# Kernel optimization log

Hardware: AMD Instinct MI355X
Metric: run time of the kernel (lower is better)

## Reference

```python
import jax, jax.numpy as jnp
import numpy as np

B, S, D, K, T = 8, 1024, 128, 16, 8  # batch, seq_len, dim, stack_size, recursion depth
N = B * S                            # per-token stack memory batch
RESIDUAL = 0.1                       # cfg.RESIDUAL_WEIGHT
EPS = 1e-6                           # cfg.EPSILON
SCALE = D ** -0.5


def _clinear(zr, zi, Wr, Wi):
    # (zr + i*zi) @ (Wr + i*Wi); W stored [in, out] (torch Linear weight transposed)
    return zr @ Wr - zi @ Wi, zi @ Wr + zr @ Wi


def _cattn(zr, zi, p):
    # ComplexAttention: complex q/k/v, softmax over concat([real, imag]) scores
    Wqr, Wqi, Wkr, Wki, Wvr, Wvi = p
    qr, qi = _clinear(zr, zi, Wqr, Wqi)
    kr, ki = _clinear(zr, zi, Wkr, Wki)
    vr, vi = _clinear(zr, zi, Wvr, Wvi)
    qf = jnp.concatenate([qr, qi], -1)
    kf = jnp.concatenate([kr, ki], -1)
    a = jax.nn.softmax(jnp.einsum('...id,...jd->...ij', qf, kf) * SCALE, -1)
    return jnp.einsum('...ij,...jd->...id', a, vr), jnp.einsum('...ij,...jd->...id', a, vi)


def setup_inputs() -> dict:
    key = jax.random.key(0)
    ks = jax.random.split(key, 18)
    mk = lambda k: jax.random.normal(k, (D, D), jnp.float32) * (D ** -0.5)
    inp = {
        'x_real': jax.random.normal(ks[0], (B, S, D), jnp.float32),
        'x_imag': jax.random.normal(ks[1], (B, S, D), jnp.float32),
        # sequence ComplexAttention weights
        'Wq_r': mk(ks[2]), 'Wq_i': mk(ks[3]),
        'Wk_r': mk(ks[4]), 'Wk_i': mk(ks[5]),
        'Wv_r': mk(ks[6]), 'Wv_i': mk(ks[7]),
        # stack-memory ComplexAttention weights
        'Mq_r': mk(ks[8]), 'Mq_i': mk(ks[9]),
        'Mk_r': mk(ks[10]), 'Mk_i': mk(ks[11]),
        'Mv_r': mk(ks[12]), 'Mv_i': mk(ks[13]),
        # ctrl projection (push/pop/stay logits) and output modulus projection
        'Wc': jax.random.normal(ks[14], (2 * D, 3), jnp.float32) * 0.05,
        'bc': jnp.zeros((3,), jnp.float32),
        'Wo': jax.random.normal(ks[15], (2 * D, D), jnp.float32) * ((2 * D) ** -0.5),
        'bo': jnp.zeros((D,), jnp.float32),
    }
    return inp


def reference(x_real, x_imag, Wq_r, Wq_i, Wk_r, Wk_i, Wv_r, Wv_i,
              Mq_r, Mq_i, Mk_r, Mk_i, Mv_r, Mv_i, Wc, bc, Wo, bo):
    seq_p = (Wq_r, Wq_i, Wk_r, Wk_i, Wv_r, Wv_i)
    mem_p = (Mq_r, Mq_i, Mk_r, Mk_i, Mv_r, Mv_i)
    mem0 = jnp.zeros((N, K, 2 * D), x_real.dtype)
    ptr0 = jnp.zeros((N, K), x_real.dtype).at[:, 0].set(1.0)  # pointer starts at slot 0

    def step(carry, _):
        zr, zi, mem, ptr = carry
        ar, ai = _cattn(zr, zi, seq_p)                         # [B,S,D] complex attention
        zf = jnp.concatenate([ar.reshape(N, D), ai.reshape(N, D)], -1)  # [N,2D]
        # gated push/pop/stay (sigmoid, then normalized as in DifferentiableStackMemory)
        g = jax.nn.sigmoid(zf @ Wc + bc)                       # [N,3]
        tot = g.sum(-1, keepdims=True) + EPS
        push, pop, stay = g[:, 0:1] / tot, g[:, 1:2] / tot, g[:, 2:3] / tot
        new_ptr = push * jnp.roll(ptr, 1, 1) + pop * jnp.roll(ptr, -1, 1) + stay * ptr
        mem = mem * (1.0 - push[..., None]) + push[..., None] * zf[:, None, :]  # gated write
        mr, mi = _cattn(mem[..., :D], mem[..., D:], mem_p)     # attention over K stack slots
        read = (jnp.concatenate([mr, mi], -1) * new_ptr[..., None]).sum(1)      # pointer-weighted read [N,2D]
        zr2 = ar + RESIDUAL * read[:, :D].reshape(B, S, D)
        zi2 = ai + RESIDUAL * read[:, D:].reshape(B, S, D)
        return (zr2, zi2, mem, new_ptr), None

    (zr, zi, _, _), _ = jax.lax.scan(step, (x_real, x_imag, mem0, ptr0), None, length=T)
    # ComplexModulusProjection: Linear(2*dim -> dim) on concat([real, imag])
    return jnp.concatenate([zr, zi], -1) @ Wo + bo
```

## Files before the change

### kernel.cpp

```cpp
#include <hip/hip_runtime.h>
#include <stdint.h>

typedef __attribute__((ext_vector_type(4))) float f32x4;

constexpr float QK_SCALE = 0.08838834764831845f;

#define DEV static __device__ __forceinline__

DEV float rdl(float v, int l){
  union { float f; int i; } u; u.f = v;
  u.i = __builtin_amdgcn_readlane(u.i, l);
  return u.f;
}


__global__ void k_init32(const float* __restrict__ xr, const float* __restrict__ xi,
                         float* __restrict__ Z, float* __restrict__ Mm,
                         float* __restrict__ PSUM){
  for (int i = blockIdx.x*blockDim.x + threadIdx.x; i < 8192*256; i += gridDim.x*blockDim.x){
    int n = i >> 8, d = i & 255;
    Z[i]  = (d < 128) ? xr[n*128 + d] : xi[n*128 + d - 128];
    Mm[i] = 0.f;
    if (i < 8192) PSUM[i] = 1.f;
  }
}

template<int EPI, int BM>
__launch_bounds__(256, 2)
__global__ void k_gemm32(const float* __restrict__ A, int nb,
                         const float* __restrict__ W0r, const float* __restrict__ W0i,
                         const float* __restrict__ W1r, const float* __restrict__ W1i,
                         const float* __restrict__ W2r, const float* __restrict__ W2i,
                         float* __restrict__ C, const float* __restrict__ PSUM,
                         const float* __restrict__ bias){
  constexpr int RM = BM / 16;
  __shared__ float As[32][BM + 4];
  __shared__ float Bs[32][132];
  const int bx = blockIdx.x % nb, by = blockIdx.x / nb;
  const int m0 = by * BM, n0 = bx << 7;
  const int tid = threadIdx.x;
  const int tx = tid & 15, ty = tid >> 4;
  const float* Wr = W0r; const float* Wi = W0i;
  if constexpr (EPI == 0){
    int sec = n0 >> 8;
    Wr = (sec == 0) ? W0r : (sec == 1) ? W1r : W2r;
    Wi = (sec == 0) ? W0i : (sec == 1) ? W1i : W2i;
  }
  const int hn = (n0 >> 7) & 1;
  float acc[RM][8];
  #pragma unroll
  for (int i = 0; i < RM; ++i)
    #pragma unroll
    for (int j = 0; j < 8; ++j) acc[i][j] = 0.f;

  for (int kt = 0; kt < 8; ++kt){
    if (kt) __syncthreads();
    #pragma unroll
    for (int i = 0; i < BM/32; ++i){
      int c = i*256 + tid;
      int row = c >> 3, k4 = c & 7;
      f32x4 v = *(const f32x4*)&A[(size_t)(m0 + row)*256 + kt*32 + k4*4];
      As[k4*4+0][row] = v.x; As[k4*4+1][row] = v.y;
      As[k4*4+2][row] = v.z; As[k4*4+3][row] = v.w;
    }
    #pragma unroll
    for (int i = 0; i < 4; ++i){
      int c = i*256 + tid;
      int k = c >> 5, n4 = c & 31;
      int gk = kt*32 + k;
      f32x4 v;
      if constexpr (EPI == 2){
        v = *(const f32x4*)&W0r[(size_t)gk*128 + n4*4];
      } else {
        int hk = gk >> 7, kk = gk & 127;
        const float* src = ((hk ^ hn) == 0) ? Wr : Wi;
        v = *(const f32x4*)&src[(size_t)kk*128 + n4*4];
        if (hk == 1 && hn == 0){ v.x = -v.x; v.y = -v.y; v.z = -v.z; v.w = -v.w; }
      }
      *(f32x4*)&Bs[k][n4*4] = v;
    }
    __syncthreads();
    #pragma unroll 8
    for (int k = 0; k < 32; ++k){
      float a[RM], b[8];
      #pragma unroll
      for (int i4 = 0; i4 < RM/4; ++i4)
        *(f32x4*)&a[i4*4] = *(const f32x4*)&As[k][ty*RM + i4*4];
      *(f32x4*)&b[0] = *(const f32x4*)&Bs[k][tx*8];
      *(f32x4*)&b[4] = *(const f32x4*)&Bs[k][tx*8 + 4];
      #pragma unroll
      for (int i = 0; i < RM; ++i)
        #pragma unroll
        for (int j = 0; j < 8; ++j) acc[i][j] += a[i]*b[j];
    }
  }
  #pragma unroll
  for (int i = 0; i < RM; ++i){
    const int row = m0 + ty*RM + i;
    const int col = n0 + tx*8;
    if constexpr (EPI == 0){
      *(f32x4*)&C[(size_t)row*768 + col]     = *(const f32x4*)&acc[i][0];
      *(f32x4*)&C[(size_t)row*768 + col + 4] = *(const f32x4*)&acc[i][4];
    } else if constexpr (EPI == 1){
      const float s = 0.1f * PSUM[row];
      f32x4 z0 = *(const f32x4*)&C[(size_t)row*256 + col];
      f32x4 z1 = *(const f32x4*)&C[(size_t)row*256 + col + 4];
      z0.x += s*acc[i][0]; z0.y += s*acc[i][1]; z0.z += s*acc[i][2]; z0.w += s*acc[i][3];
      z1.x += s*acc[i][4]; z1.y += s*acc[i][5]; z1.z += s*acc[i][6]; z1.w += s*acc[i][7];
      *(f32x4*)&C[(size_t)row*256 + col]     = z0;
      *(f32x4*)&C[(size_t)row*256 + col + 4] = z1;
    } else {
      f32x4 b0 = *(const f32x4*)&bias[col];
      f32x4 b1 = *(const f32x4*)&bias[col + 4];
      f32x4 o0 = {acc[i][0]+b0.x, acc[i][1]+b0.y, acc[i][2]+b0.z, acc[i][3]+b0.w};
      f32x4 o1 = {acc[i][4]+b1.x, acc[i][5]+b1.y, acc[i][6]+b1.z, acc[i][7]+b1.w};
      *(f32x4*)&C[(size_t)row*128 + col]     = o0;
      *(f32x4*)&C[(size_t)row*128 + col + 4] = o1;
    }
  }
}

__launch_bounds__(512, 1)
__global__ void k_attn32(const float* __restrict__ QKV, float* __restrict__ ZF,
                         float* __restrict__ Mm, float* __restrict__ PSUM,
                         const float* __restrict__ Wc, const float* __restrict__ bc){
  __shared__ __align__(16) float KV[16*260];
  const int tid = threadIdx.x;
  const int tx = tid & 63;
  const int ty = tid >> 6;
  const int batch = blockIdx.x >> 5, qt = blockIdx.x & 31;
  const int nbase = batch*1024 + qt*32;
  const int kv0 = batch*1024;

  float qreg[4][4];
  #pragma unroll
  for (int r = 0; r < 4; ++r)
    #pragma unroll
    for (int g = 0; g < 4; ++g)
      qreg[r][g] = QKV[(size_t)(nbase + ty*4 + r)*768 + g*64 + tx];

  float O[4][4];
  #pragma unroll
  for (int r = 0; r < 4; ++r)
    #pragma unroll
    for (int j = 0; j < 4; ++j) O[r][j] = 0.f;
  float mr[4] = {-3.0e30f, -3.0e30f, -3.0e30f, -3.0e30f};
  float lr[4] = {0.f, 0.f, 0.f, 0.f};

  for (int t = 0; t < 4; ++t){
    const int kb = kv0 + t*256;
    float S[4][4];
    #pragma unroll
    for (int r = 0; r < 4; ++r)
      #pragma unroll
      for (int e = 0; e < 4; ++e) S[r][e] = 0.f;

    #pragma unroll
    for (int gg = 0; gg < 4; ++gg){
      for (int dcc = 0; dcc < 4; ++dcc){
        const int dc = gg*4 + dcc;
        __syncthreads();
        #pragma unroll
        for (int i = 0; i < 2; ++i){
          const int c = i*512 + tid;
          const int key = c & 255, d4 = c >> 8;
          f32x4 v = *(const f32x4*)&QKV[(size_t)(kb + key)*768 + 256 + dc*16 + d4*4];
          KV[(d4*4+0)*260 + key] = v.x; KV[(d4*4+1)*260 + key] = v.y;
          KV[(d4*4+2)*260 + key] = v.z; KV[(d4*4+3)*260 + key] = v.w;
        }
        __syncthreads();
        #pragma unroll
        for (int k = 0; k < 16; ++k){
          const int ln = dcc*16 + k;
          const float a0 = rdl(qreg[0][gg], ln);
          const float a1 = rdl(qreg[1][gg], ln);
          const float a2 = rdl(qreg[2][gg], ln);
          const float a3 = rdl(qreg[3][gg], ln);
          const f32x4 b = *(const f32x4*)&KV[k*260 + tx*4];
          S[0][0] += a0*b.x; S[0][1] += a0*b.y; S[0][2] += a0*b.z; S[0][3] += a0*b.w;
          S[1][0] += a1*b.x; S[1][1] += a1*b.y; S[1][2] += a1*b.z; S[1][3] += a1*b.w;
          S[2][0] += a2*b.x; S[2][1] += a2*b.y; S[2][2] += a2*b.z; S[2][3] += a2*b.w;
          S[3][0] += a3*b.x; S[3][1] += a3*b.y; S[3][2] += a3*b.z; S[3][3] += a3*b.w;
        }
      }
    }
    float pp[4][4];
    #pragma unroll
    for (int r = 0; r < 4; ++r){
      #pragma unroll
      for (int e = 0; e < 4; ++e) S[r][e] *= QK_SCALE;
      float tm = fmaxf(fmaxf(S[r][0], S[r][1]), fmaxf(S[r][2], S[r][3]));
      tm = fmaxf(tm, __shfl_xor(tm, 1));
      tm = fmaxf(tm, __shfl_xor(tm, 2));
      tm = fmaxf(tm, __shfl_xor(tm, 4));
      tm = fmaxf(tm, __shfl_xor(tm, 8));
      tm = fmaxf(tm, __shfl_xor(tm, 16));
      tm = fmaxf(tm, __shfl_xor(tm, 32));
      const float mn = fmaxf(mr[r], tm);
      const float al = expf(mr[r] - mn);
      pp[r][0] = expf(S[r][0] - mn); pp[r][1] = expf(S[r][1] - mn);
      pp[r][2] = expf(S[r][2] - mn); pp[r][3] = expf(S[r][3] - mn);
      float rs = (pp[r][0] + pp[r][1]) + (pp[r][2] + pp[r][3]);
      rs += __shfl_xor(rs, 1); rs += __shfl_xor(rs, 2);
      rs += __shfl_xor(rs, 4); rs += __shfl_xor(rs, 8);
      rs += __shfl_xor(rs, 16); rs += __shfl_xor(rs, 32);
      lr[r] = lr[r]*al + rs;
      mr[r] = mn;
      O[r][0] *= al; O[r][1] *= al; O[r][2] *= al; O[r][3] *= al;
    }
    for (int ks = 0; ks < 16; ++ks){
      __syncthreads();
      #pragma unroll
      for (int i = 0; i < 2; ++i){
        const int c = i*512 + tid;
        const int key = c >> 6, d4 = c & 63;
        *(f32x4*)&KV[key*260 + d4*4] =
            *(const f32x4*)&QKV[(size_t)(kb + ks*16 + key)*768 + 512 + d4*4];
      }
      __syncthreads();
      #pragma unroll
      for (int kg = 0; kg < 4; ++kg){
        const int ln = ks*4 + kg;
        #pragma unroll
        for (int k2 = 0; k2 < 4; ++k2){
          const float a0 = rdl(pp[0][k2], ln);
          const float a1 = rdl(pp[1][k2], ln);
          const float a2 = rdl(pp[2][k2], ln);
          const float a3 = rdl(pp[3][k2], ln);
          const f32x4 v = *(const f32x4*)&KV[(kg*4+k2)*260 + tx*4];
          O[0][0] += a0*v.x; O[0][1] += a0*v.y; O[0][2] += a0*v.z; O[0][3] += a0*v.w;
          O[1][0] += a1*v.x; O[1][1] += a1*v.y; O[1][2] += a1*v.z; O[1][3] += a1*v.w;
          O[2][0] += a2*v.x; O[2][1] += a2*v.y; O[2][2] += a2*v.z; O[2][3] += a2*v.w;
          O[3][0] += a3*v.x; O[3][1] += a3*v.y; O[3][2] += a3*v.z; O[3][3] += a3*v.w;
        }
      }
    }
  }
  const float bc0 = bc[0], bc1 = bc[1], bc2 = bc[2];
  #pragma unroll
  for (int r = 0; r < 4; ++r){
    const float inv = 1.f / lr[r];
    #pragma unroll
    for (int j = 0; j < 4; ++j) O[r][j] *= inv;
    float d0 = 0.f, d1 = 0.f, d2 = 0.f;
    #pragma unroll
    for (int j = 0; j < 4; ++j){
      const int dim = tx*4 + j;
      const float z = O[r][j];
      d0 += z*Wc[dim*3 + 0]; d1 += z*Wc[dim*3 + 1]; d2 += z*Wc[dim*3 + 2];
    }
    d0 += __shfl_xor(d0,1); d0 += __shfl_xor(d0,2); d0 += __shfl_xor(d0,4);
    d0 += __shfl_xor(d0,8); d0 += __shfl_xor(d0,16); d0 += __shfl_xor(d0,32);
    d1 += __shfl_xor(d1,1); d1 += __shfl_xor(d1,2); d1 += __shfl_xor(d1,4);
    d1 += __shfl_xor(d1,8); d1 += __shfl_xor(d1,16); d1 += __shfl_xor(d1,32);
    d2 += __shfl_xor(d2,1); d2 += __shfl_xor(d2,2); d2 += __shfl_xor(d2,4);
    d2 += __shfl_xor(d2,8); d2 += __shfl_xor(d2,16); d2 += __shfl_xor(d2,32);
    const float g0 = 1.f/(1.f + expf(-(d0 + bc0)));
    const float g1 = 1.f/(1.f + expf(-(d1 + bc1)));
    const float g2 = 1.f/(1.f + expf(-(d2 + bc2)));
    const float tt = g0 + g1 + g2, tot = tt + 1e-6f;
    const float push = g0/tot;
    const int row = nbase + ty*4 + r;
    if (tx == 0) PSUM[row] *= tt/tot;
    const size_t idx = (size_t)row*256 + tx*4;
    f32x4 z0 = {O[r][0], O[r][1], O[r][2], O[r][3]};
    f32x4 m0 = *(const f32x4*)&Mm[idx];
    m0.x += push*(z0.x - m0.x); m0.y += push*(z0.y - m0.y);
    m0.z += push*(z0.z - m0.z); m0.w += push*(z0.w - m0.w);
    *(f32x4*)&Mm[idx] = m0;
    *(f32x4*)&ZF[idx] = z0;
  }
}

extern "C" void kernel_launch(void* const* d_in, const int* in_sizes, int n_in,
                              void* d_out, int out_size, void* d_ws, size_t ws_size,
                              hipStream_t stream){
  (void)in_sizes; (void)n_in; (void)out_size; (void)ws_size;
  const float* xr   = (const float*)d_in[0];
  const float* xi   = (const float*)d_in[1];
  const float* Wq_r = (const float*)d_in[2];
  const float* Wq_i = (const float*)d_in[3];
  const float* Wk_r = (const float*)d_in[4];
  const float* Wk_i = (const float*)d_in[5];
  const float* Wv_r = (const float*)d_in[6];
  const float* Wv_i = (const float*)d_in[7];
  const float* Mv_r = (const float*)d_in[12];
  const float* Mv_i = (const float*)d_in[13];
  const float* Wc   = (const float*)d_in[14];
  const float* bc   = (const float*)d_in[15];
  const float* Wo   = (const float*)d_in[16];
  const float* bo   = (const float*)d_in[17];

  uint8_t* w = (uint8_t*)d_ws;
  float* Z    = (float*)w; w += (size_t)8192*256*4;
  float* QKV  = (float*)w; w += (size_t)8192*768*4;
  float* Mm   = (float*)w; w += (size_t)8192*256*4;
  float* PSUM = (float*)w; w += (size_t)8192*4;
  float* ZF   = Z;

  k_init32<<<dim3(1024), dim3(256), 0, stream>>>(xr, xi, Z, Mm, PSUM);
  for (int t = 0; t < 8; ++t){
    k_gemm32<0,64><<<dim3(768), dim3(256), 0, stream>>>(Z, 6,
        Wq_r, Wq_i, Wk_r, Wk_i, Wv_r, Wv_i, QKV, nullptr, nullptr);
    k_attn32<<<dim3(256), dim3(512), 0, stream>>>(QKV, ZF, Mm, PSUM, Wc, bc);
    k_gemm32<1,64><<<dim3(256), dim3(256), 0, stream>>>(Mm, 2,
        Mv_r, Mv_i, nullptr, nullptr, nullptr, nullptr, Z, PSUM, nullptr);
  }
  k_gemm32<2,128><<<dim3(64), dim3(256), 0, stream>>>(Z, 1,
      Wo, nullptr, nullptr, nullptr, nullptr, nullptr, (float*)d_out, nullptr, bo);
}
```

Measured before the change: 2.112 ms.

## Double-buffer K/V shared-memory tiles in sequence attention kernel

The K and V staging buffers in the sequence attention kernel become two shared-memory buffers. Each step now writes the next K or V tile into the other buffer while computing on the current one, which replaces two barriers per tile with one. The stages are chained across the QK, PV and next-tile phases. This aims to overlap global loads with FMA work and cut sync stalls, at the cost of double the shared memory and more complex buffer-parity logic.

```diff
diff --git a/kernel.cpp b/kernel.cpp
--- a/kernel.cpp
+++ b/kernel.cpp
@@ -124,7 +124,7 @@
 __global__ void k_attn32(const float* __restrict__ QKV, float* __restrict__ ZF,
                          float* __restrict__ Mm, float* __restrict__ PSUM,
                          const float* __restrict__ Wc, const float* __restrict__ bc){
-  __shared__ __align__(16) float KV[16*260];
+  __shared__ __align__(16) float KV[2][16*260];
   const int tid = threadIdx.x;
   const int tx = tid & 63;
   const int ty = tid >> 6;
@@ -132,6 +132,9 @@
   const int nbase = batch*1024 + qt*32;
   const int kv0 = batch*1024;
 
+  const int sK_key = tid & 255,  sK_d4 = tid >> 8;
+  const int sV_key0 = tid >> 6,  sV_d4 = tid & 63;
+
   float qreg[4][4];
   #pragma unroll
   for (int r = 0; r < 4; ++r)
@@ -147,6 +150,27 @@
   float mr[4] = {-3.0e30f, -3.0e30f, -3.0e30f, -3.0e30f};
   float lr[4] = {0.f, 0.f, 0.f, 0.f};
 
+  #define STAGE_K(kb, dc, b)                                                   \
+    { _Pragma("unroll")                                                        \
+      for (int i = 0; i < 2; ++i){                                             \
+        const int key = sK_key, d4 = sK_d4 + i*2;                              \
+        f32x4 v = *(const f32x4*)&QKV[(size_t)((kb) + key)*768 + 256 + (dc)*16 + d4*4]; \
+        float* dst = &KV[b][0];                                                \
+        dst[(d4*4+0)*260 + key] = v.x; dst[(d4*4+1)*260 + key] = v.y;          \
+        dst[(d4*4+2)*260 + key] = v.z; dst[(d4*4+3)*260 + key] = v.w;          \
+      } }
+  #define STAGE_V(kb, ks, b)                                                   \
+    { _Pragma("unroll")                                                        \
+      for (int i = 0; i < 2; ++i){                                             \
+        const int key = sV_key0 + i*8, d4 = sV_d4;                             \
+        *(f32x4*)&KV[b][key*260 + d4*4] =                                      \
+            *(const f32x4*)&QKV[(size_t)((kb) + (ks)*16 + key)*768 + 512 + d4*4]; \
+      } }
+
+  const int kb0 = kv0;
+  STAGE_K(kb0, 0, 0);
+  __syncthreads();
+
   for (int t = 0; t < 4; ++t){
     const int kb = kv0 + t*256;
     float S[4][4];
@@ -159,16 +183,9 @@
     for (int gg = 0; gg < 4; ++gg){
       for (int dcc = 0; dcc < 4; ++dcc){
         const int dc = gg*4 + dcc;
-        __syncthreads();
-        #pragma unroll
-        for (int i = 0; i < 2; ++i){
-          const int c = i*512 + tid;
-          const int key = c & 255, d4 = c >> 8;
-          f32x4 v = *(const f32x4*)&QKV[(size_t)(kb + key)*768 + 256 + dc*16 + d4*4];
-          KV[(d4*4+0)*260 + key] = v.x; KV[(d4*4+1)*260 + key] = v.y;
-          KV[(d4*4+2)*260 + key] = v.z; KV[(d4*4+3)*260 + key] = v.w;
-        }
-        __syncthreads();
+        if (dc < 15){ STAGE_K(kb, dc + 1, (dc + 1) & 1); }
+        else        { STAGE_V(kb, 0, 0); }
+        const float* buf = &KV[dc & 1][0];
         #pragma unroll
         for (int k = 0; k < 16; ++k){
           const int ln = dcc*16 + k;
@@ -176,12 +193,13 @@
           const float a1 = rdl(qreg[1][gg], ln);
           const float a2 = rdl(qreg[2][gg], ln);
           const float a3 = rdl(qreg[3][gg], ln);
-          const f32x4 b = *(const f32x4*)&KV[k*260 + tx*4];
+          const f32x4 b = *(const f32x4*)&buf[k*260 + tx*4];
           S[0][0] += a0*b.x; S[0][1] += a0*b.y; S[0][2] += a0*b.z; S[0][3] += a0*b.w;
           S[1][0] += a1*b.x; S[1][1] += a1*b.y; S[1][2] += a1*b.z; S[1][3] += a1*b.w;
           S[2][0] += a2*b.x; S[2][1] += a2*b.y; S[2][2] += a2*b.z; S[2][3] += a2*b.w;
           S[3][0] += a3*b.x; S[3][1] += a3*b.y; S[3][2] += a3*b.z; S[3][3] += a3*b.w;
         }
+        __syncthreads();
       }
     }
     float pp[4][4];
@@ -209,15 +227,9 @@
       O[r][0] *= al; O[r][1] *= al; O[r][2] *= al; O[r][3] *= al;
     }
     for (int ks = 0; ks < 16; ++ks){
-      __syncthreads();
-      #pragma unroll
-      for (int i = 0; i < 2; ++i){
-        const int c = i*512 + tid;
-        const int key = c >> 6, d4 = c & 63;
-        *(f32x4*)&KV[key*260 + d4*4] =
-            *(const f32x4*)&QKV[(size_t)(kb + ks*16 + key)*768 + 512 + d4*4];
-      }
-      __syncthreads();
+      if (ks < 15)      { STAGE_V(kb, ks + 1, (ks + 1) & 1); }
+      else if (t < 3)   { STAGE_K(kb + 256, 0, 0); }
+      const float* buf = &KV[ks & 1][0];
       #pragma unroll
       for (int kg = 0; kg < 4; ++kg){
         const int ln = ks*4 + kg;
@@ -227,15 +239,18 @@
           const float a1 = rdl(pp[1][k2], ln);
           const float a2 = rdl(pp[2][k2], ln);
           const float a3 = rdl(pp[3][k2], ln);
-          const f32x4 v = *(const f32x4*)&KV[(kg*4+k2)*260 + tx*4];
+          const f32x4 v = *(const f32x4*)&buf[(kg*4+k2)*260 + tx*4];
           O[0][0] += a0*v.x; O[0][1] += a0*v.y; O[0][2] += a0*v.z; O[0][3] += a0*v.w;
           O[1][0] += a1*v.x; O[1][1] += a1*v.y; O[1][2] += a1*v.z; O[1][3] += a1*v.w;
           O[2][0] += a2*v.x; O[2][1] += a2*v.y; O[2][2] += a2*v.z; O[2][3] += a2*v.w;
           O[3][0] += a3*v.x; O[3][1] += a3*v.y; O[3][2] += a3*v.z; O[3][3] += a3*v.w;
         }
       }
-    }
-  }
+      __syncthreads();
+    }
+  }
+  #undef STAGE_K
+  #undef STAGE_V
   const float bc0 = bc[0], bc1 = bc[1], bc2 = bc[2];
   #pragma unroll
   for (int r = 0; r < 4; ++r){
```

New measurement: 3.737 ms. +76.9%, slower.
